# Kernel optimization log

Hardware: AMD Instinct MI355X
Metric: run time of the kernel (lower is better)

The kernel has to match this reference:

```python
import jax, jax.numpy as jnp
from jax import lax
import numpy as np

HIDDEN = 40
NUM_LAYERS = 7
B, H, W = 16, 64, 64
KS = 7
PAD = KS // 2  # 3

# mask for conv_2d type 'A': zero rows below center, zero right-of-center in
# the center row, and zero the center tap itself
_m = np.ones((1, 1, KS, KS), np.float32)
_m[:, :, PAD + 1:, :] = 0
_m[:, :, PAD, PAD + 1:] = 0
_m[:, :, PAD, PAD] = 0
MASK_A = jnp.asarray(_m)


def conv2d(x, w, pad):
    return lax.conv_general_dilated(x, w, (1, 1), pad,
                                    dimension_numbers=('NCHW', 'OIHW', 'NCHW'))


def setup_inputs() -> dict:
    key = jax.random.key(0)
    ks = jax.random.split(key, 12)
    s = 0.05
    return {
        'input_tensor': jax.random.normal(ks[0], (B, 1, H, W), jnp.float32),
        'target_tensor': jax.random.normal(ks[1], (B, 1, H, W), jnp.float32),
        # masked conv_2d(7,1,80) applied to target
        'w_is': jax.random.normal(ks[2], (2 * HIDDEN, 1, KS, KS), jnp.float32) * s,
        'b_is': jnp.ones((2 * HIDDEN,), jnp.float32),
        # conv_i_s: Conv2d(1, 80, 7, pad 3)
        'w_cis': jax.random.normal(ks[3], (2 * HIDDEN, 1, KS, KS), jnp.float32) * s,
        'b_cis': jax.random.normal(ks[4], (2 * HIDDEN,), jnp.float32) * s,
        # row convs: Conv2d(40, 40, [1,3], pad [0,1])
        'w_rh': jax.random.normal(ks[5], (HIDDEN, HIDDEN, 1, 3), jnp.float32) * s,
        'b_rh': jax.random.normal(ks[6], (HIDDEN,), jnp.float32) * s,
        'w_rc': jax.random.normal(ks[7], (HIDDEN, HIDDEN, 1, 3), jnp.float32) * s,
        'b_rc': jax.random.normal(ks[8], (HIDDEN,), jnp.float32) * s,
        # per-layer cell 1x1 convs: 40 -> 160, stacked over layers
        'w_cell': jax.random.normal(ks[9], (NUM_LAYERS, 4 * HIDDEN, HIDDEN), jnp.float32) * s,
        'b_cell': jax.random.normal(ks[10], (NUM_LAYERS, 4 * HIDDEN), jnp.float32) * s,
        # conv_out: Conv2d(40, 256, 1)
        'w_out': jax.random.normal(ks[11], (256, HIDDEN), jnp.float32) * s,
        'b_out': jnp.zeros((256,), jnp.float32),
    }


def reference(input_tensor, target_tensor, w_is, b_is, w_cis, b_cis,
              w_rh, b_rh, w_rc, b_rc, w_cell, b_cell, w_out, b_out):
    same7 = ((PAD, PAD), (PAD, PAD))
    # i_s = cat([conv_i_s(input), masked_conv(target)], dim=1) -> [B, 160, H, W]
    i_s_input = conv2d(input_tensor, w_cis, same7) + b_cis[None, :, None, None]
    i_s_target = conv2d(target_tensor, w_is * MASK_A, same7) + b_is[None, :, None, None]
    i_s = jnp.concatenate([i_s_input, i_s_target], axis=1)

    h0 = jnp.zeros((B, HIDDEN, 1, W), i_s.dtype)
    c0 = jnp.zeros((B, HIDDEN, 1, W), i_s.dtype)

    def step(carry, x_t):  # x_t: [B, 160, 1, W]
        h, c = carry
        h = conv2d(h, w_rh, ((0, 0), (1, 1))) + b_rh[None, :, None, None]
        c = conv2d(c, w_rc, ((0, 0), (1, 1))) + b_rc[None, :, None, None]
        for l in range(NUM_LAYERS):
            h_conv = jnp.einsum('oc,bcrw->borw', w_cell[l], h) + b_cell[l][None, :, None, None]
            combined = x_t + h_conv
            cc_i, cc_f, cc_o, cc_g = jnp.split(combined, 4, axis=1)
            i = jax.nn.sigmoid(cc_i)
            f = jax.nn.sigmoid(cc_f)
            o = jax.nn.sigmoid(cc_o)
            g = jnp.tanh(cc_g)
            c = f * c + i * g
            h = o * jnp.tanh(c)
        return (h, c), h

    xs = jnp.moveaxis(i_s, 2, 0)[:, :, :, None, :]  # [H, B, 160, 1, W]
    _, hs = lax.scan(step, (h0, c0), xs)            # hs: [H, B, 40, 1, W]
    hidden = jnp.moveaxis(hs[:, :, :, 0, :], 0, 2)  # [B, 40, H, W]
    out = jnp.einsum('oc,bchw->bohw', w_out, hidden) + b_out[None, :, None, None]
    return jax.nn.relu(out)
```

## Files before the change

kernel.cpp:

```cpp
#include <hip/hip_runtime.h>


typedef __bf16 bf16x8 __attribute__((ext_vector_type(8)));
typedef __bf16 bf16x4 __attribute__((ext_vector_type(4)));
typedef float  f32x4  __attribute__((ext_vector_type(4)));

#define SC1 (-1.44269504089f)
#define SC2 (-2.88539008178f)

#define STP 56
#define HLS 896
#define CWS 17

#define BARRIER_LGKM() __asm__ volatile("s_waitcnt lgkmcnt(0)\ns_barrier" ::: "memory")

__global__ __launch_bounds__(256) void prep_kernel(
        const float* __restrict__ wcell, const float* __restrict__ wrh,
        const float* __restrict__ wrc, const float* __restrict__ bcell,
        const float* __restrict__ brh, const float* __restrict__ brc,
        __bf16* __restrict__ wsA) {
    int i = blockIdx.x * 256 + threadIdx.x;
    if (i >= 90112) return;
    float val = 0.0f;
    if (i < 35840) {
        int j = i & 7, lane = (i >> 3) & 63, lm = i >> 9;
        int mt = lm % 10, l = lm / 10;
        int k = (lane >> 4) * 8 + j, m = lane & 15, r = m & 3;
        int row = r * 40 + 4 * mt + (m >> 2);
        val = wcell[(l * 160 + row) * 40 + k] * (r == 3 ? SC2 : SC1);
    } else if (i < 71680) {
        int i2 = i - 35840;
        int j = i2 & 7, lane = (i2 >> 3) & 63, lm = i2 >> 9;
        int mt = lm % 10, l = lm / 10;
        int k = 32 + (lane >> 4) * 8 + j, m = lane & 15, r = m & 3;
        int row = r * 40 + 4 * mt + (m >> 2);
        float s = (r == 3 ? SC2 : SC1);
        if (k < 40)       val = wcell[(l * 160 + row) * 40 + k] * s;
        else if (k == 40) val = bcell[l * 160 + row] * s;
    } else if (i < 80896) {
        int i3 = i - 71680;
        int j = i3 & 7, lane = (i3 >> 3) & 63, idx = i3 >> 9;
        int mtc = idx % 3, t2 = idx / 3, dx = t2 % 3, cv = t2 / 3;
        int k = (lane >> 4) * 8 + j;
        int ch = 16 * mtc + (lane & 15);
        const float* w = cv ? wrc : wrh;
        if (ch < 40) val = w[(ch * 40 + k) * 3 + dx];
    } else {
        int i4 = i - 80896;
        int j = i4 & 7, lane = (i4 >> 3) & 63, idx = i4 >> 9;
        int mtc = idx % 3, t2 = idx / 3, dx = t2 % 3, cv = t2 / 3;
        int k = 32 + (lane >> 4) * 8 + j;
        int ch = 16 * mtc + (lane & 15);
        if (ch < 40) {
            const float* w = cv ? wrc : wrh;
            if (k < 40)                    val = w[(ch * 40 + k) * 3 + dx];
            else if (k == 40 && dx == 1)   val = (cv ? brc : brh)[ch];
        }
    }
    wsA[i] = (__bf16)val;
}

__global__ __launch_bounds__(256) void conv7_kernel(
        const float* __restrict__ inp, const float* __restrict__ tgt,
        const float* __restrict__ w_is, const float* __restrict__ b_is,
        const float* __restrict__ w_cis, const float* __restrict__ b_cis,
        float* __restrict__ x_ws) {
    int b = blockIdx.x >> 6, y = blockIdx.x & 63;
    int tid = threadIdx.x, qq = tid >> 6, w = tid & 63;
    const float* ib = inp + b * 4096;
    const float* tb = tgt + b * 4096;
    float pin[7][7], ptg[4][7];
#pragma unroll
    for (int dy = 0; dy < 7; dy++) {
        int yy = y + dy - 3;
#pragma unroll
        for (int dx = 0; dx < 7; dx++) {
            int xx = w + dx - 3;
            bool ok = (yy >= 0 && yy < 64 && xx >= 0 && xx < 64);
            pin[dy][dx] = ok ? ib[yy * 64 + xx] : 0.0f;
            if (dy < 4) ptg[dy][dx] = ok ? tb[yy * 64 + xx] : 0.0f;
        }
    }
    int g = w >> 4, l16 = w & 15;
    for (int j = 0; j < 10; j++) {
        int cc = 4 * j + qq;
        int ccu = __builtin_amdgcn_readfirstlane(cc);
        float a0 = b_cis[ccu], a1 = b_cis[40 + ccu];
        float a2 = b_is[ccu], a3 = b_is[40 + ccu];
        const float* w0 = w_cis + ccu * 49;
        const float* w1 = w_cis + (40 + ccu) * 49;
        const float* w2 = w_is + ccu * 49;
        const float* w3 = w_is + (40 + ccu) * 49;
#pragma unroll
        for (int dy = 0; dy < 7; dy++)
#pragma unroll
            for (int dx = 0; dx < 7; dx++) {
                a0 = __builtin_fmaf(w0[dy * 7 + dx], pin[dy][dx], a0);
                a1 = __builtin_fmaf(w1[dy * 7 + dx], pin[dy][dx], a1);
            }
#pragma unroll
        for (int dy = 0; dy < 3; dy++)
#pragma unroll
            for (int dx = 0; dx < 7; dx++) {
                a2 = __builtin_fmaf(w2[dy * 7 + dx], ptg[dy][dx], a2);
                a3 = __builtin_fmaf(w3[dy * 7 + dx], ptg[dy][dx], a3);
            }
#pragma unroll
        for (int dx = 0; dx < 3; dx++) {
            a2 = __builtin_fmaf(w2[21 + dx], ptg[3][dx], a2);
            a3 = __builtin_fmaf(w3[21 + dx], ptg[3][dx], a3);
        }
        size_t idx = (size_t)((((b * 64 + y) * 4 + g) * 10 + j) * 4 + qq) * 64
                     + l16 * 4;
        *(f32x4*)&x_ws[idx] = f32x4{a0 * SC1, a1 * SC1, a2 * SC1, a3 * SC2};
    }
}

__global__ __launch_bounds__(640, 1) void rnn_kernel(
        const float* __restrict__ x_ws, const __bf16* __restrict__ wsA,
        float* __restrict__ hid_ws,
        unsigned long long* __restrict__ halo_ws) {
    __shared__ __align__(16) __bf16 hC[18 * STP + 64];
    __shared__ __align__(16) __bf16 cC[18 * STP + 64];
    __shared__ __align__(16) __bf16 hL[2 * HLS + 32];
    __shared__ float cwf[40 * CWS];

    const int bid = blockIdx.x, g = bid >> 4, b = bid & 15;
    const int tid = threadIdx.x, wv = tid >> 6, lane = tid & 63;
    const int q = lane >> 4, l16 = lane & 15, cc = 4 * wv + q;
    const int W0 = g * 16;

    for (int i = tid; i < 536; i += 640) {
        ((float*)hC)[i] = 0.0f;
        ((float*)cC)[i] = 0.0f;
    }
    for (int i = tid; i < 912; i += 640)
        ((float*)hL)[i] = 0.0f;
    for (int i = tid; i < 40 * CWS; i += 640) cwf[i] = 0.0f;
    __syncthreads();
    if (tid < 18) { hC[tid * STP + 40] = (__bf16)1.0f; cC[tid * STP + 40] = (__bf16)1.0f; }
    if (tid < 32) hL[(tid >> 4) * HLS + (tid & 15) * STP + 40] = (__bf16)1.0f;
    __syncthreads();

    bf16x8 a0c[7], a1c[7];
#pragma unroll
    for (int l = 0; l < 7; l++) {
        a0c[l] = *(const bf16x8*)&wsA[((l * 10 + wv) * 64 + lane) * 8];
        a1c[l] = *(const bf16x8*)&wsA[35840 + ((l * 10 + wv) * 64 + lane) * 8];
    }
    bf16x8 cva0[3], cva1[3];
    {
        int cv = (wv < 3) ? 0 : 1, mtc = (wv < 3) ? wv : wv - 3;
        int sel = (wv < 6) ? (cv * 3) : 0;
#pragma unroll
        for (int dx = 0; dx < 3; dx++) {
            int it = ((sel + dx) * 3 + ((wv < 6) ? mtc : 0));
            cva0[dx] = *(const bf16x8*)&wsA[71680 + (it * 64 + lane) * 8];
            cva1[dx] = *(const bf16x8*)&wsA[80896 + (it * 64 + lane) * 8];
        }
    }

    float c_reg = 0.0f;
    const size_t xstride = 10240;
    const size_t xbase0 = (size_t)(b * 64) * xstride
        + (((size_t)g * 10 + wv) * 4 + q) * 64 + l16 * 4;
    f32x4 xv = *(const f32x4*)&x_ws[xbase0];

    for (int t = 0; t < 64; t++) {
        f32x4 xn = xv;
        if (t < 63) xn = *(const f32x4*)&x_ws[xbase0 + (size_t)(t + 1) * xstride];

        if (wv < 6) {
            const __bf16* st = (wv < 3) ? hC : cC;
            f32x4 acc = f32x4{0.f, 0.f, 0.f, 0.f};
#pragma unroll
            for (int dx = 0; dx < 3; dx++) {
                bf16x8 b0 = *(const bf16x8*)&st[(l16 + dx) * STP + q * 8];
                bf16x8 b1 = *(const bf16x8*)&st[(l16 + dx) * STP + 32 + q * 8];
                acc = __builtin_amdgcn_mfma_f32_16x16x32_bf16(cva0[dx], b0, acc, 0, 0, 0);
                acc = __builtin_amdgcn_mfma_f32_16x16x32_bf16(cva1[dx], b1, acc, 0, 0, 0);
            }
            int mtc = (wv < 3) ? wv : wv - 3;
            int ch0 = 16 * mtc + 4 * q;
            if (ch0 < 40) {
                if (wv < 3) {
                    bf16x4 hv;
#pragma unroll
                    for (int r = 0; r < 4; r++) hv[r] = (__bf16)acc[r];
                    *(bf16x4*)&hL[l16 * STP + ch0] = hv;
                } else {
#pragma unroll
                    for (int r = 0; r < 4; r++) cwf[(ch0 + r) * CWS + l16] = acc[r];
                }
            }
        }
        BARRIER_LGKM();

#pragma unroll
        for (int l = 0; l < 7; l++) {
            const __bf16* hb = &hL[(l & 1) * HLS];
            bf16x8 b0 = *(const bf16x8*)&hb[l16 * STP + q * 8];
            bf16x8 b1 = *(const bf16x8*)&hb[l16 * STP + 32 + q * 8];
            f32x4 acc = __builtin_amdgcn_mfma_f32_16x16x32_bf16(
                a0c[l], b0, f32x4{0.f, 0.f, 0.f, 0.f}, 0, 0, 0);
            acc = __builtin_amdgcn_mfma_f32_16x16x32_bf16(a1c[l], b1, acc, 0, 0, 0);
            if (l == 0) c_reg = cwf[cc * CWS + l16];
            float Ei = __builtin_amdgcn_exp2f(fminf(acc[0] + xv[0], 44.f));
            float Ef = __builtin_amdgcn_exp2f(fminf(acc[1] + xv[1], 44.f));
            float Eo = __builtin_amdgcn_exp2f(fminf(acc[2] + xv[2], 44.f));
            float Eg = __builtin_amdgcn_exp2f(fminf(acc[3] + xv[3], 44.f));
            float f = __builtin_amdgcn_rcpf(1.0f + Ef);
            float ig = (1.0f - Eg) * __builtin_amdgcn_rcpf((1.0f + Ei) * (1.0f + Eg));
            float c = __builtin_fmaf(f, c_reg, ig);
            c_reg = c;
            float Ec = __builtin_amdgcn_exp2f(fminf(SC2 * c, 44.f));
            float h = (1.0f - Ec) * __builtin_amdgcn_rcpf((1.0f + Eo) * (1.0f + Ec));
            if (l < 6) {
                hL[((l + 1) & 1) * HLS + l16 * STP + cc] = (__bf16)h;
                BARRIER_LGKM();
            } else {
                hC[(l16 + 1) * STP + cc] = (__bf16)h;
                cC[(l16 + 1) * STP + cc] = (__bf16)c;
                hid_ws[(size_t)((b * 64 + t) * 40 + cc) * 64 + W0 + l16] = h;
                if (t < 63) {
                    unsigned short h16 = __builtin_bit_cast(unsigned short, (__bf16)h);
                    unsigned short c16 = __builtin_bit_cast(unsigned short, (__bf16)c);
                    unsigned long long v = ((unsigned long long)(unsigned)t << 32)
                        | ((unsigned)c16 << 16) | (unsigned)h16;
                    if (l16 == 0 && g > 0)
                        __hip_atomic_store(
                            &halo_ws[((bid * 2 + 0) * 2 + (t & 1)) * 40 + cc], v,
                            __ATOMIC_RELAXED, __HIP_MEMORY_SCOPE_AGENT);
                    if (l16 == 15 && g < 3)
                        __hip_atomic_store(
                            &halo_ws[((bid * 2 + 1) * 2 + (t & 1)) * 40 + cc], v,
                            __ATOMIC_RELAXED, __HIP_MEMORY_SCOPE_AGENT);
                }
            }
        }

        if (t < 63) {
            if (wv == 8 && g > 0 && lane < 40) {
                const unsigned long long* src =
                    &halo_ws[(((bid - 16) * 2 + 1) * 2 + (t & 1)) * 40 + lane];
                unsigned long long v = __hip_atomic_load(
                    src, __ATOMIC_RELAXED, __HIP_MEMORY_SCOPE_AGENT);
                while ((unsigned)(v >> 32) != (unsigned)t) {
                    __builtin_amdgcn_s_sleep(1);
                    v = __hip_atomic_load(src, __ATOMIC_RELAXED,
                                          __HIP_MEMORY_SCOPE_AGENT);
                }
                hC[lane] = __builtin_bit_cast(__bf16, (unsigned short)(v & 0xffffu));
                cC[lane] = __builtin_bit_cast(__bf16, (unsigned short)((v >> 16) & 0xffffu));
            }
            if (wv == 9 && g < 3 && lane < 40) {
                const unsigned long long* src =
                    &halo_ws[(((bid + 16) * 2 + 0) * 2 + (t & 1)) * 40 + lane];
                unsigned long long v = __hip_atomic_load(
                    src, __ATOMIC_RELAXED, __HIP_MEMORY_SCOPE_AGENT);
                while ((unsigned)(v >> 32) != (unsigned)t) {
                    __builtin_amdgcn_s_sleep(1);
                    v = __hip_atomic_load(src, __ATOMIC_RELAXED,
                                          __HIP_MEMORY_SCOPE_AGENT);
                }
                hC[17 * STP + lane] = __builtin_bit_cast(__bf16, (unsigned short)(v & 0xffffu));
                cC[17 * STP + lane] = __builtin_bit_cast(__bf16, (unsigned short)((v >> 16) & 0xffffu));
            }
        }
        BARRIER_LGKM();
        xv = xn;
    }
}

__global__ __launch_bounds__(256) void out_kernel(
        const float* __restrict__ hid_ws, const float* __restrict__ w_out,
        const float* __restrict__ b_out, float* __restrict__ out) {
    __shared__ float wlds[40 * 264];
    __shared__ float hlds[40 * 64];
    int b = blockIdx.x >> 6, y = blockIdx.x & 63;
    int tid = threadIdx.x;
    for (int i = tid; i < 10240; i += 256) {
        int o = i / 40, k = i - o * 40;
        wlds[k * 264 + o] = w_out[i];
    }
    const float* hbp = hid_ws + (size_t)(b * 64 + y) * 40 * 64;
    for (int i = tid; i < 2560; i += 256) hlds[i] = hbp[i];
    __syncthreads();

    int tn = tid & 7, tm = tid >> 3;
    int wbase = tn * 8, obase = tm * 8;
    float acc[8][8];
#pragma unroll
    for (int io = 0; io < 8; io++)
#pragma unroll
        for (int iw = 0; iw < 8; iw++) acc[io][iw] = 0.0f;

    for (int k = 0; k < 40; k++) {
        f32x4 hA = *(const f32x4*)&hlds[k * 64 + wbase];
        f32x4 hB = *(const f32x4*)&hlds[k * 64 + wbase + 4];
        f32x4 wA = *(const f32x4*)&wlds[k * 264 + obase];
        f32x4 wB = *(const f32x4*)&wlds[k * 264 + obase + 4];
#pragma unroll
        for (int io = 0; io < 8; io++) {
            float wo = (io < 4) ? wA[io] : wB[io - 4];
#pragma unroll
            for (int iw = 0; iw < 8; iw++) {
                float hx = (iw < 4) ? hA[iw] : hB[iw - 4];
                acc[io][iw] = __builtin_fmaf(wo, hx, acc[io][iw]);
            }
        }
    }
#pragma unroll
    for (int io = 0; io < 8; io++) {
        int o = obase + io;
        float bo = b_out[o];
        f32x4 s0, s1;
#pragma unroll
        for (int iw = 0; iw < 4; iw++)
            s0[iw] = fmaxf(acc[io][iw] + bo, 0.0f);
#pragma unroll
        for (int iw = 0; iw < 4; iw++)
            s1[iw] = fmaxf(acc[io][iw + 4] + bo, 0.0f);
        float* ob = out + (size_t)((b * 256 + o) * 64 + y) * 64 + wbase;
        *(f32x4*)ob = s0;
        *(f32x4*)(ob + 4) = s1;
    }
}

extern "C" void kernel_launch(void* const* d_in, const int* in_sizes, int n_in,
                              void* d_out, int out_size, void* d_ws,
                              size_t ws_size, hipStream_t stream) {
    const float* input  = (const float*)d_in[0];
    const float* target = (const float*)d_in[1];
    const float* w_is   = (const float*)d_in[2];
    const float* b_is   = (const float*)d_in[3];
    const float* w_cis  = (const float*)d_in[4];
    const float* b_cis  = (const float*)d_in[5];
    const float* w_rh   = (const float*)d_in[6];
    const float* b_rh   = (const float*)d_in[7];
    const float* w_rc   = (const float*)d_in[8];
    const float* b_rc   = (const float*)d_in[9];
    const float* w_cell = (const float*)d_in[10];
    const float* b_cell = (const float*)d_in[11];
    const float* w_out  = (const float*)d_in[12];
    const float* b_out  = (const float*)d_in[13];
    float* out = (float*)d_out;

    char* ws = (char*)d_ws;
    float*              x_ws    = (float*)ws;
    float*              hid_ws  = (float*)(ws + 41943040);
    __bf16*             wsA     = (__bf16*)(ws + 52428800);
    unsigned long long* halo_ws = (unsigned long long*)(ws + 52609024);

    prep_kernel<<<352, 256, 0, stream>>>(w_cell, w_rh, w_rc, b_cell, b_rh,
                                         b_rc, wsA);
    conv7_kernel<<<1024, 256, 0, stream>>>(input, target, w_is, b_is, w_cis,
                                           b_cis, x_ws);
    rnn_kernel<<<64, 640, 0, stream>>>(x_ws, wsA, hid_ws, halo_ws);
    out_kernel<<<1024, 256, 0, stream>>>(hid_ws, w_out, b_out, out);
}
```

Measured before the change: 373.9 us.

## Fold row-h conv into layer-0 cell weights and replace barrier with LDS flags

Precomputes the product of layer-0 cell weights and the h row-conv weights (plus folded biases) in the prep kernel. Every wave can then compute layer-0 gate preactivations directly from hC with 6 MFMAs, skipping the separate h-conv stage and its hL store. The full workgroup barrier before the layer loop becomes per-tile LDS flags set by the c-conv waves, with other waves spin-waiting only on the flag they need. This aims to shorten the serial per-timestep critical path. In exchange it adds extra MFMAs per wave, spin-wait overhead, and a bf16 rounding of the fused weights.

```diff
diff --git a/kernel.cpp b/kernel.cpp
--- a/kernel.cpp
+++ b/kernel.cpp
@@ -20,7 +20,7 @@
         const float* __restrict__ brh, const float* __restrict__ brc,
         __bf16* __restrict__ wsA) {
     int i = blockIdx.x * 256 + threadIdx.x;
-    if (i >= 90112) return;
+    if (i >= 120832) return;
     float val = 0.0f;
     if (i < 35840) {
         int j = i & 7, lane = (i >> 3) & 63, lm = i >> 9;
@@ -45,7 +45,7 @@
         int ch = 16 * mtc + (lane & 15);
         const float* w = cv ? wrc : wrh;
         if (ch < 40) val = w[(ch * 40 + k) * 3 + dx];
-    } else {
+    } else if (i < 90112) {
         int i4 = i - 80896;
         int j = i4 & 7, lane = (i4 >> 3) & 63, idx = i4 >> 9;
         int mtc = idx % 3, t2 = idx / 3, dx = t2 % 3, cv = t2 / 3;
@@ -55,6 +55,37 @@
             const float* w = cv ? wrc : wrh;
             if (k < 40)                    val = w[(ch * 40 + k) * 3 + dx];
             else if (k == 40 && dx == 1)   val = (cv ? brc : brh)[ch];
+        }
+    } else if (i < 105472) {
+        int i5 = i - 90112;
+        int j = i5 & 7, lane = (i5 >> 3) & 63, idx = i5 >> 9;
+        int mt = idx % 10, dx = idx / 10;
+        int k = (lane >> 4) * 8 + j, m = lane & 15, r = m & 3;
+        int row = r * 40 + 4 * mt + (m >> 2);
+        float s = (r == 3 ? SC2 : SC1);
+        float acc = 0.0f;
+        for (int mm = 0; mm < 40; mm++)
+            acc = __builtin_fmaf(wcell[row * 40 + mm],
+                                 wrh[(mm * 40 + k) * 3 + dx], acc);
+        val = acc * s;
+    } else {
+        int i6 = i - 105472;
+        int j = i6 & 7, lane = (i6 >> 3) & 63, idx = i6 >> 9;
+        int mt = idx % 10, dx = idx / 10;
+        int k = 32 + (lane >> 4) * 8 + j, m = lane & 15, r = m & 3;
+        int row = r * 40 + 4 * mt + (m >> 2);
+        float s = (r == 3 ? SC2 : SC1);
+        if (k < 40) {
+            float acc = 0.0f;
+            for (int mm = 0; mm < 40; mm++)
+                acc = __builtin_fmaf(wcell[row * 40 + mm],
+                                     wrh[(mm * 40 + k) * 3 + dx], acc);
+            val = acc * s;
+        } else if (k == 40 && dx == 1) {
+            float acc = bcell[row];
+            for (int mm = 0; mm < 40; mm++)
+                acc = __builtin_fmaf(wcell[row * 40 + mm], brh[mm], acc);
+            val = acc * s;
         }
     }
     wsA[i] = (__bf16)val;
@@ -124,6 +155,7 @@
     __shared__ __align__(16) __bf16 cC[18 * STP + 64];
     __shared__ __align__(16) __bf16 hL[2 * HLS + 32];
     __shared__ float cwf[40 * CWS];
+    __shared__ unsigned cflag[4];
 
     const int bid = blockIdx.x, g = bid >> 4, b = bid & 15;
     const int tid = threadIdx.x, wv = tid >> 6, lane = tid & 63;
@@ -137,24 +169,30 @@
     for (int i = tid; i < 912; i += 640)
         ((float*)hL)[i] = 0.0f;
     for (int i = tid; i < 40 * CWS; i += 640) cwf[i] = 0.0f;
+    if (tid < 4) cflag[tid] = 0xFFFFFFFFu;
     __syncthreads();
     if (tid < 18) { hC[tid * STP + 40] = (__bf16)1.0f; cC[tid * STP + 40] = (__bf16)1.0f; }
     if (tid < 32) hL[(tid >> 4) * HLS + (tid & 15) * STP + 40] = (__bf16)1.0f;
     __syncthreads();
 
-    bf16x8 a0c[7], a1c[7];
-#pragma unroll
-    for (int l = 0; l < 7; l++) {
-        a0c[l] = *(const bf16x8*)&wsA[((l * 10 + wv) * 64 + lane) * 8];
-        a1c[l] = *(const bf16x8*)&wsA[35840 + ((l * 10 + wv) * 64 + lane) * 8];
+    bf16x8 a0c[6], a1c[6];
+#pragma unroll
+    for (int l = 1; l < 7; l++) {
+        a0c[l - 1] = *(const bf16x8*)&wsA[((l * 10 + wv) * 64 + lane) * 8];
+        a1c[l - 1] = *(const bf16x8*)&wsA[35840 + ((l * 10 + wv) * 64 + lane) * 8];
+    }
+    bf16x8 f0c[3], f1c[3];
+#pragma unroll
+    for (int dx = 0; dx < 3; dx++) {
+        f0c[dx] = *(const bf16x8*)&wsA[90112 + ((dx * 10 + wv) * 64 + lane) * 8];
+        f1c[dx] = *(const bf16x8*)&wsA[105472 + ((dx * 10 + wv) * 64 + lane) * 8];
     }
     bf16x8 cva0[3], cva1[3];
-    {
-        int cv = (wv < 3) ? 0 : 1, mtc = (wv < 3) ? wv : wv - 3;
-        int sel = (wv < 6) ? (cv * 3) : 0;
+    if (wv >= 3 && wv < 6) {
+        int mtc = wv - 3;
 #pragma unroll
         for (int dx = 0; dx < 3; dx++) {
-            int it = ((sel + dx) * 3 + ((wv < 6) ? mtc : 0));
+            int it = (3 + dx) * 3 + mtc;
             cva0[dx] = *(const bf16x8*)&wsA[71680 + (it * 64 + lane) * 8];
             cva1[dx] = *(const bf16x8*)&wsA[80896 + (it * 64 + lane) * 8];
         }
@@ -170,41 +208,56 @@
         f32x4 xn = xv;
         if (t < 63) xn = *(const f32x4*)&x_ws[xbase0 + (size_t)(t + 1) * xstride];
 
-        if (wv < 6) {
-            const __bf16* st = (wv < 3) ? hC : cC;
-            f32x4 acc = f32x4{0.f, 0.f, 0.f, 0.f};
+        if (wv >= 3 && wv < 6) {
+            f32x4 ac = f32x4{0.f, 0.f, 0.f, 0.f};
 #pragma unroll
             for (int dx = 0; dx < 3; dx++) {
-                bf16x8 b0 = *(const bf16x8*)&st[(l16 + dx) * STP + q * 8];
-                bf16x8 b1 = *(const bf16x8*)&st[(l16 + dx) * STP + 32 + q * 8];
-                acc = __builtin_amdgcn_mfma_f32_16x16x32_bf16(cva0[dx], b0, acc, 0, 0, 0);
-                acc = __builtin_amdgcn_mfma_f32_16x16x32_bf16(cva1[dx], b1, acc, 0, 0, 0);
-            }
-            int mtc = (wv < 3) ? wv : wv - 3;
-            int ch0 = 16 * mtc + 4 * q;
+                bf16x8 b0 = *(const bf16x8*)&cC[(l16 + dx) * STP + q * 8];
+                bf16x8 b1 = *(const bf16x8*)&cC[(l16 + dx) * STP + 32 + q * 8];
+                ac = __builtin_amdgcn_mfma_f32_16x16x32_bf16(cva0[dx], b0, ac, 0, 0, 0);
+                ac = __builtin_amdgcn_mfma_f32_16x16x32_bf16(cva1[dx], b1, ac, 0, 0, 0);
+            }
+            int mtc = wv - 3, ch0 = 16 * mtc + 4 * q;
             if (ch0 < 40) {
-                if (wv < 3) {
-                    bf16x4 hv;
-#pragma unroll
-                    for (int r = 0; r < 4; r++) hv[r] = (__bf16)acc[r];
-                    *(bf16x4*)&hL[l16 * STP + ch0] = hv;
-                } else {
-#pragma unroll
-                    for (int r = 0; r < 4; r++) cwf[(ch0 + r) * CWS + l16] = acc[r];
-                }
-            }
-        }
-        BARRIER_LGKM();
+#pragma unroll
+                for (int r = 0; r < 4; r++) cwf[(ch0 + r) * CWS + l16] = ac[r];
+            }
+            __asm__ volatile("s_waitcnt lgkmcnt(0)" ::: "memory");
+            if (lane == 0)
+                __hip_atomic_store(&cflag[mtc], (unsigned)t,
+                                   __ATOMIC_RELAXED, __HIP_MEMORY_SCOPE_WORKGROUP);
+        }
+
+        f32x4 acc0 = f32x4{0.f, 0.f, 0.f, 0.f};
+#pragma unroll
+        for (int dx = 0; dx < 3; dx++) {
+            bf16x8 b0 = *(const bf16x8*)&hC[(l16 + dx) * STP + q * 8];
+            bf16x8 b1 = *(const bf16x8*)&hC[(l16 + dx) * STP + 32 + q * 8];
+            acc0 = __builtin_amdgcn_mfma_f32_16x16x32_bf16(f0c[dx], b0, acc0, 0, 0, 0);
+            acc0 = __builtin_amdgcn_mfma_f32_16x16x32_bf16(f1c[dx], b1, acc0, 0, 0, 0);
+        }
+        {
+            int jj = wv >> 2;
+            while (__hip_atomic_load(&cflag[jj], __ATOMIC_RELAXED,
+                                     __HIP_MEMORY_SCOPE_WORKGROUP) != (unsigned)t)
+                __builtin_amdgcn_s_sleep(1);
+            __asm__ volatile("" ::: "memory");
+        }
 
 #pragma unroll
         for (int l = 0; l < 7; l++) {
-            const __bf16* hb = &hL[(l & 1) * HLS];
-            bf16x8 b0 = *(const bf16x8*)&hb[l16 * STP + q * 8];
-            bf16x8 b1 = *(const bf16x8*)&hb[l16 * STP + 32 + q * 8];
-            f32x4 acc = __builtin_amdgcn_mfma_f32_16x16x32_bf16(
-                a0c[l], b0, f32x4{0.f, 0.f, 0.f, 0.f}, 0, 0, 0);
-            acc = __builtin_amdgcn_mfma_f32_16x16x32_bf16(a1c[l], b1, acc, 0, 0, 0);
-            if (l == 0) c_reg = cwf[cc * CWS + l16];
+            f32x4 acc;
+            if (l == 0) {
+                acc = acc0;
+                c_reg = cwf[cc * CWS + l16];
+            } else {
+                const __bf16* hb = &hL[(l & 1) * HLS];
+                bf16x8 b0 = *(const bf16x8*)&hb[l16 * STP + q * 8];
+                bf16x8 b1 = *(const bf16x8*)&hb[l16 * STP + 32 + q * 8];
+                acc = __builtin_amdgcn_mfma_f32_16x16x32_bf16(
+                    a0c[l - 1], b0, f32x4{0.f, 0.f, 0.f, 0.f}, 0, 0, 0);
+                acc = __builtin_amdgcn_mfma_f32_16x16x32_bf16(a1c[l - 1], b1, acc, 0, 0, 0);
+            }
             float Ei = __builtin_amdgcn_exp2f(fminf(acc[0] + xv[0], 44.f));
             float Ef = __builtin_amdgcn_exp2f(fminf(acc[1] + xv[1], 44.f));
             float Eo = __builtin_amdgcn_exp2f(fminf(acc[2] + xv[2], 44.f));
@@ -350,9 +403,9 @@
     float*              x_ws    = (float*)ws;
     float*              hid_ws  = (float*)(ws + 41943040);
     __bf16*             wsA     = (__bf16*)(ws + 52428800);
-    unsigned long long* halo_ws = (unsigned long long*)(ws + 52609024);
-
-    prep_kernel<<<352, 256, 0, stream>>>(w_cell, w_rh, w_rc, b_cell, b_rh,
+    unsigned long long* halo_ws = (unsigned long long*)(ws + 52670464);
+
+    prep_kernel<<<472, 256, 0, stream>>>(w_cell, w_rh, w_rc, b_cell, b_rh,
                                          b_rc, wsA);
     conv7_kernel<<<1024, 256, 0, stream>>>(input, target, w_is, b_is, w_cis,
                                            b_cis, x_ws);
```

Measured after the change: 369.4 us. No clear change (-1.2%).
